# Performance work log

Hardware: AMD Instinct MI355X
Metric: run time of the kernel (lower is better)

Reference implementation:

```python
import jax, jax.numpy as jnp
import numpy as np

B, T, D_MODEL, N_HEADS = 2, 2048, 1024, 16
HEAD_DIM = D_MODEL // N_HEADS
GN_EPS = 1e-5


def decay_gammas(n_heads):
    # gamma_h = 1 - 2^(-5 - h*(8/n_heads))
    h = jnp.arange(n_heads, dtype=jnp.float32)
    return 1.0 - jnp.power(2.0, -5.0 - h * (8.0 / n_heads))


def setup_inputs() -> dict:
    key = jax.random.key(0)
    ks = jax.random.split(key, 7)
    w_scale = 0.02
    return {
        "x": jax.random.normal(ks[0], (B, T, D_MODEL), dtype=jnp.float32),
        "Wq": jax.random.normal(ks[1], (D_MODEL, D_MODEL), dtype=jnp.float32) * w_scale,
        "Wk": jax.random.normal(ks[2], (D_MODEL, D_MODEL), dtype=jnp.float32) * w_scale,
        "Wv": jax.random.normal(ks[3], (D_MODEL, D_MODEL), dtype=jnp.float32) * w_scale,
        "Wo": jax.random.normal(ks[4], (D_MODEL, D_MODEL), dtype=jnp.float32) * w_scale,
        "gn_w": jnp.ones((D_MODEL,), dtype=jnp.float32),
        "gn_b": jnp.zeros((D_MODEL,), dtype=jnp.float32),
    }


def reference(x, Wq, Wk, Wv, Wo, gn_w, gn_b):
    Bx, Tx, C = x.shape
    H, D = N_HEADS, C // N_HEADS
    gammas = decay_gammas(H)  # (H,)

    def split_heads(y):
        return y.reshape(Bx, Tx, H, D).transpose(0, 2, 1, 3)  # (B,H,T,D)

    # torch Linear: y = x @ W.T
    Q = split_heads(x @ Wq.T)
    K = split_heads(x @ Wk.T)
    V = split_heads(x @ Wv.T)

    # causal decay mask D[h,i,j] = gamma_h^(i-j) if i>=j else 0
    idx = jnp.arange(Tx, dtype=jnp.float32)
    diff = idx[:, None] - idx[None, :]  # (T,T)
    mask = jnp.where(diff >= 0,
                     gammas[:, None, None] ** jnp.maximum(diff, 0.0),
                     0.0)  # (H,T,T)

    scores = jnp.einsum("bhtd,bhsd->bhts", Q, K) / jnp.sqrt(jnp.float32(D))
    scores = scores * mask[None]  # (B,H,T,T)
    out = jnp.einsum("bhts,bhsd->bhtd", scores, V)  # (B,H,T,D)
    y = out.transpose(0, 2, 1, 3).reshape(Bx, Tx, C)  # merge heads

    # GroupNorm(n_heads, d_model) applied on (B, C, T): normalizes over
    # (head_dim, T) per group per batch element.
    z = y.transpose(0, 2, 1).reshape(Bx, H, D, Tx)
    mu = z.mean(axis=(2, 3), keepdims=True)
    var = z.var(axis=(2, 3), keepdims=True)
    zn = (z - mu) * jax.lax.rsqrt(var + GN_EPS)
    zn = zn * gn_w.reshape(1, H, D, 1) + gn_b.reshape(1, H, D, 1)
    y = zn.reshape(Bx, C, Tx).transpose(0, 2, 1)  # (B,T,C)

    return y @ Wo.T
```

## Files before the change

### kernel.cpp

```cpp
#include <hip/hip_runtime.h>
#include <hip/hip_bf16.h>

typedef __attribute__((ext_vector_type(8))) short short8;
typedef __attribute__((ext_vector_type(4))) float float4v;
typedef __attribute__((ext_vector_type(16))) float float16v;
typedef unsigned short u16;
typedef unsigned long long ull;

#define KD 1024

__device__ __forceinline__ u16 f2b(float f) {
    __hip_bfloat16 h = __float2bfloat16(f);
    return __builtin_bit_cast(u16, h);
}
__device__ __forceinline__ float b2f(u16 u) {
    unsigned x = ((unsigned)u) << 16;
    return __builtin_bit_cast(float, x);
}
__device__ __forceinline__ float lg_gamma(int h) {
    float gamma = 1.0f - exp2f(-5.0f - 0.5f * (float)h);
    return log2f(gamma);
}

__device__ __forceinline__ void async_cp16(const u16* g, u16* l) {
    __builtin_amdgcn_global_load_lds(
        (const __attribute__((address_space(1))) void*)g,
        (__attribute__((address_space(3))) void*)l,
        16, 0, 0);
}

__global__ __launch_bounds__(256)
void cvt_all(const float* __restrict__ x, const float* __restrict__ wq,
             const float* __restrict__ wk, const float* __restrict__ wv,
             const float* __restrict__ wo,
             u16* __restrict__ xb, u16* __restrict__ wqkvb, u16* __restrict__ wob)
{
    int bid = blockIdx.x;
    if (bid < 4096) {
        long i = (long)bid * 1024 + threadIdx.x * 4;
        float4 v = *(const float4*)(x + i);
        ushort4 u;
        u.x = f2b(v.x); u.y = f2b(v.y); u.z = f2b(v.z); u.w = f2b(v.w);
        *(ushort4*)(xb + i) = u;
    } else {
        int wbid = bid - 4096;
        int mtx = wbid >> 10;
        int n = wbid & 1023;
        const float* src = (mtx == 0) ? wq : (mtx == 1) ? wk : (mtx == 2) ? wv : wo;
        u16* dst = (mtx == 3) ? wob : (wqkvb + (size_t)mtx * 1048576);
        float sc = (mtx == 0) ? 0.125f : 1.0f;
        int k0 = threadIdx.x * 4;
        float4 v = *(const float4*)(src + (size_t)n * 1024 + k0);
        int panel = n >> 5, row = n & 31, kg = k0 >> 4, kh = (k0 >> 3) & 1, off = k0 & 7;
        size_t o = (size_t)panel * 32768 + (size_t)kg * 512 + kh * 256 + row * 8 + off;
        ushort4 u;
        u.x = f2b(v.x * sc); u.y = f2b(v.y * sc); u.z = f2b(v.z * sc); u.w = f2b(v.w * sc);
        *(ushort4*)(dst + o) = u;
    }
}

template<int MODE>
__global__ __launch_bounds__(256)
void gemm_nt(const u16* __restrict__ A, const u16* __restrict__ Bpk,
             u16* __restrict__ oQ, u16* __restrict__ oK,
             u16* __restrict__ oKt, u16* __restrict__ oVt,
             float* __restrict__ of)
{
    constexpr int TM = (MODE == 0) ? 128 : 64;
    constexpr int MI = (MODE == 0) ? 2 : 1;
    __shared__ __attribute__((aligned(16))) u16 Sh[(MODE == 0) ? 16384 : 4096];
    u16* As = Sh;
    const int tid = threadIdx.x;
    const int lane = tid & 63;
    const int wv = tid >> 6;
    const int wm = wv >> 1, wn = wv & 1;
    const int row32 = lane & 31, khalf = lane >> 5;
    const int lrow = lane >> 3, lseg = lane & 7;
    const int lin = blockIdx.x + gridDim.x * blockIdx.y;
    const int xcd = lin & 7, idx = lin >> 3;
    int m_tile, n_tile;
    if (MODE == 0) { m_tile = (idx & 3) + 4 * xcd; n_tile = idx >> 2; }
    else           { m_tile = (idx & 7) + 8 * xcd; n_tile = idx >> 3; }
    const int m0 = m_tile * TM, n0 = n_tile * 128;

    float16v acc[MI][2];
#pragma unroll
    for (int i = 0; i < MI; i++)
#pragma unroll
        for (int j = 0; j < 2; j++)
#pragma unroll
            for (int r = 0; r < 16; r++) acc[i][j][r] = 0.f;

    const int scol = (lseg ^ lrow) << 3;
    const u16* bp = Bpk + (size_t)((n0 >> 5) + wn * 2) * 32768 + (size_t)lane * 8;

    for (int kt = 0; kt < KD; kt += 64) {
        __syncthreads();
#pragma unroll
        for (int i = 0; i < TM / 32; i++) {
            int r = wv * (TM / 4) + i * 8;
            async_cp16(A + (size_t)(m0 + r + lrow) * KD + kt + scol, &As[r * 64]);
        }
        short8 bgl[4][2];
#pragma unroll
        for (int ks = 0; ks < 4; ks++)
#pragma unroll
            for (int j = 0; j < 2; j++)
                bgl[ks][j] = *(const short8*)(bp + (size_t)j * 32768 + ((kt >> 4) + ks) * 512);
        __syncthreads();
#pragma unroll
        for (int ks = 0; ks < 4; ks++) {
            short8 af[MI];
#pragma unroll
            for (int i = 0; i < MI; i++) {
                int row = wm * (MI * 32) + i * 32 + row32;
                af[i] = *(const short8*)(&As[row * 64 + (((ks * 2 + khalf) ^ (row & 7)) << 3)]);
            }
#pragma unroll
            for (int i = 0; i < MI; i++)
#pragma unroll
                for (int j = 0; j < 2; j++)
                    acc[i][j] = __builtin_amdgcn_mfma_f32_32x32x16_bf16(af[i], bgl[ks][j], acc[i][j], 0, 0, 0);
        }
    }

    if (MODE == 0) {
        const int wsel = n0 >> 10;
        if (wsel <= 1) {
            u16* dst = (wsel == 0) ? oQ : oK;
#pragma unroll
            for (int i = 0; i < 2; i++)
#pragma unroll
                for (int j = 0; j < 2; j++) {
                    int gn = n0 + wn * 64 + j * 32 + row32;
                    int dd = gn & 63, hh = (gn >> 6) & 15;
#pragma unroll
                    for (int reg = 0; reg < 16; reg++) {
                        int m = m0 + wm * 64 + i * 32 + (reg & 3) + 8 * (reg >> 2) + 4 * khalf;
                        int b = m >> 11, t = m & 2047;
                        dst[(size_t)(b * 16 + hh) * 131072 + t * 64 + dd] = f2b(acc[i][j][reg]);
                    }
                }
        }
        if (wsel >= 1) {
            __syncthreads();
            u16* Tl = Sh + wv * 4096;
#pragma unroll
            for (int i = 0; i < 2; i++)
#pragma unroll
                for (int j = 0; j < 2; j++) {
                    int n_loc = j * 32 + row32;
#pragma unroll
                    for (int g = 0; g < 4; g++) {
                        int m4 = i * 32 + 8 * g + 4 * khalf;
                        ull pk = (ull)f2b(acc[i][j][4 * g]) | ((ull)f2b(acc[i][j][4 * g + 1]) << 16) |
                                 ((ull)f2b(acc[i][j][4 * g + 2]) << 32) | ((ull)f2b(acc[i][j][4 * g + 3]) << 48);
                        *(ull*)(&Tl[n_loc * 64 + (((m4 >> 3) ^ (n_loc & 7)) << 3) + (m4 & 7)]) = pk;
                    }
                }
            __syncthreads();
            int gnb = n0 + wn * 64;
            int hh = (gnb >> 6) & 15;
            int mb = m0 + wm * 64;
            int bh = (mb >> 11) * 16 + hh;
            int t0 = mb & 2047;
            u16* dstT = (wsel == 1) ? oKt : oVt;
            int rr = lane >> 3, ss = lane & 7;
#pragma unroll
            for (int g = 0; g < 8; g++) {
                int row = 8 * g + rr;
                short8 v = *(const short8*)(&Tl[row * 64 + ((ss ^ rr) << 3)]);
                *(short8*)(&dstT[(size_t)bh * 131072 + (size_t)row * 2048 + t0 + ss * 8]) = v;
            }
        }
    } else {
        int gn0 = n0 + wn * 64 + row32;
#pragma unroll
        for (int g = 0; g < 4; g++)
#pragma unroll
            for (int rr = 0; rr < 4; rr++) {
                int reg = 4 * g + rr;
                int m = m0 + wm * 32 + 8 * g + 4 * khalf + rr;
                of[(size_t)m * 1024 + gn0] = acc[0][0][reg];
                of[(size_t)m * 1024 + gn0 + 32] = acc[0][1][reg];
            }
    }
}

__global__ __launch_bounds__(256)
void chunk_state(const u16* __restrict__ Kt, const u16* __restrict__ Vt,
                 u16* __restrict__ U)
{
    const int c = blockIdx.x, bh = blockIdx.y, h = bh & 15;
    const int tid = threadIdx.x, lane = tid & 63, w = tid >> 6;
    const int row16 = lane & 15, quad = lane >> 4;
    const float lg = lg_gamma(h);
    const size_t base = (size_t)bh * 131072;

    float4v acc[4];
    float4v zero4 = {0.f, 0.f, 0.f, 0.f};
#pragma unroll
    for (int tn = 0; tn < 4; tn++) acc[tn] = zero4;

#pragma unroll
    for (int kb = 0; kb < 2; kb++) {
        short8 a = *(const short8*)(Vt + base + (size_t)(16 * w + row16) * 2048 + c * 64 + kb * 32 + quad * 8);
        short8 as;
        int e0 = 63 - (kb * 32 + quad * 8);
#pragma unroll
        for (int jj = 0; jj < 8; jj++) {
            float v = b2f((u16)a[jj]) * exp2f(lg * (float)(e0 - jj));
            as[jj] = (short)f2b(v);
        }
#pragma unroll
        for (int tn = 0; tn < 4; tn++) {
            short8 bfr = *(const short8*)(Kt + base + (size_t)(16 * tn + row16) * 2048 + c * 64 + kb * 32 + quad * 8);
            acc[tn] = __builtin_amdgcn_mfma_f32_16x16x32_bf16(as, bfr, acc[tn], 0, 0, 0);
        }
    }
    u16* up = U + ((size_t)bh * 32 + c) * 4096;
#pragma unroll
    for (int tn = 0; tn < 4; tn++)
#pragma unroll
        for (int r = 0; r < 4; r++)
            up[(16 * w + quad * 4 + r) * 64 + 16 * tn + row16] = f2b(acc[tn][r]);
}

__global__ __launch_bounds__(256)
void state_scan(const u16* __restrict__ U, u16* __restrict__ St)
{
    const int bh = blockIdx.y;
    const int e = blockIdx.x * 256 + threadIdx.x;
    const float g64 = exp2f(lg_gamma(bh & 15) * 64.0f);
    float s = 0.f;
    St[(size_t)bh * 131072 + e] = 0;
    for (int c = 1; c < 32; c++) {
        s = g64 * s + b2f(U[((size_t)bh * 32 + (c - 1)) * 4096 + e]);
        St[((size_t)bh * 32 + c) * 4096 + e] = f2b(s);
    }
}

__global__ __launch_bounds__(256)
void retention_chunk(const u16* __restrict__ Q, const u16* __restrict__ Kb,
                     const u16* __restrict__ Vt, const u16* __restrict__ St,
                     float* __restrict__ Y, float* __restrict__ stats)
{
    __shared__ __attribute__((aligned(16))) u16 Pl[4][16 * 72];
    __shared__ float red[8];
    const int c = blockIdx.x, bh = blockIdx.y, h = bh & 15;
    const int tid = threadIdx.x, lane = tid & 63, w = tid >> 6;
    const int row16 = lane & 15, quad = lane >> 4;
    const float lg = lg_gamma(h);
    const size_t base = (size_t)bh * 131072;
    float4v zero4 = {0.f, 0.f, 0.f, 0.f};

    short8 qf[2];
#pragma unroll
    for (int kb = 0; kb < 2; kb++)
        qf[kb] = *(const short8*)(Q + base + (size_t)(c * 64 + 16 * w + row16) * 64 + kb * 32 + quad * 8);

    float4v accp[4];
#pragma unroll
    for (int tn = 0; tn < 4; tn++) accp[tn] = zero4;
#pragma unroll
    for (int tn = 0; tn < 4; tn++)
#pragma unroll
        for (int kb = 0; kb < 2; kb++) {
            short8 kf = *(const short8*)(Kb + base + (size_t)(c * 64 + 16 * tn + row16) * 64 + kb * 32 + quad * 8);
            accp[tn] = __builtin_amdgcn_mfma_f32_16x16x32_bf16(qf[kb], kf, accp[tn], 0, 0, 0);
        }
#pragma unroll
    for (int tn = 0; tn < 4; tn++)
#pragma unroll
        for (int r = 0; r < 4; r++) {
            int a_loc = 16 * w + quad * 4 + r;
            int b_loc = 16 * tn + row16;
            int d = a_loc - b_loc;
            float v = (d >= 0) ? accp[tn][r] * exp2f(lg * (float)d) : 0.f;
            Pl[w][(quad * 4 + r) * 72 + b_loc] = f2b(v);
        }
    __syncthreads();

    short8 pf[2];
#pragma unroll
    for (int kb = 0; kb < 2; kb++)
        pf[kb] = *(const short8*)(&Pl[w][row16 * 72 + kb * 32 + quad * 8]);

    float4v acco[4], acci[4];
#pragma unroll
    for (int tn = 0; tn < 4; tn++) { acco[tn] = zero4; acci[tn] = zero4; }
#pragma unroll
    for (int tn = 0; tn < 4; tn++)
#pragma unroll
        for (int kb = 0; kb < 2; kb++) {
            short8 vf = *(const short8*)(Vt + base + (size_t)(16 * tn + row16) * 2048 + c * 64 + kb * 32 + quad * 8);
            acco[tn] = __builtin_amdgcn_mfma_f32_16x16x32_bf16(pf[kb], vf, acco[tn], 0, 0, 0);
            short8 sf = *(const short8*)(St + ((size_t)bh * 32 + c) * 4096 + (16 * tn + row16) * 64 + kb * 32 + quad * 8);
            acci[tn] = __builtin_amdgcn_mfma_f32_16x16x32_bf16(qf[kb], sf, acci[tn], 0, 0, 0);
        }

    float s = 0.f, s2 = 0.f;
#pragma unroll
    for (int tn = 0; tn < 4; tn++)
#pragma unroll
        for (int r = 0; r < 4; r++) {
            int a_loc = 16 * w + quad * 4 + r;
            float gi = exp2f(lg * (float)(a_loc + 1));
            int t = c * 64 + a_loc, d2 = 16 * tn + row16;
            float yv = acco[tn][r] + gi * acci[tn][r];
            Y[(size_t)bh * 131072 + t * 64 + d2] = yv;
            s += yv;
            s2 += yv * yv;
        }
#pragma unroll
    for (int off = 32; off; off >>= 1) {
        s += __shfl_down(s, off, 64);
        s2 += __shfl_down(s2, off, 64);
    }
    if (lane == 0) { red[w] = s; red[4 + w] = s2; }
    __syncthreads();
    if (tid == 0) {
        atomicAdd(&stats[2 * bh], red[0] + red[1] + red[2] + red[3]);
        atomicAdd(&stats[2 * bh + 1], red[4] + red[5] + red[6] + red[7]);
    }
}

__global__ __launch_bounds__(256)
void gn_apply(const float* __restrict__ Y, const float* __restrict__ stats,
              const float* __restrict__ gnw, const float* __restrict__ gnb,
              u16* __restrict__ Z)
{
    int i4 = (blockIdx.x * 256 + threadIdx.x) * 4;
    int b = i4 >> 21, t = (i4 >> 10) & 2047, cc = i4 & 1023;
    int hh = cc >> 6, dd = cc & 63, bh = b * 16 + hh;
    float4 v = *(const float4*)(Y + (size_t)bh * 131072 + t * 64 + dd);
    float S = stats[2 * bh], S2 = stats[2 * bh + 1];
    float mu = S * (1.0f / 131072.f);
    float var = S2 * (1.0f / 131072.f) - mu * mu;
    float rsg = rsqrtf(var + 1e-5f);
    float4 wv = *(const float4*)(gnw + cc);
    float4 bv = *(const float4*)(gnb + cc);
    ushort4 o;
    o.x = f2b((v.x - mu) * rsg * wv.x + bv.x);
    o.y = f2b((v.y - mu) * rsg * wv.y + bv.y);
    o.z = f2b((v.z - mu) * rsg * wv.z + bv.z);
    o.w = f2b((v.w - mu) * rsg * wv.w + bv.w);
    *(ushort4*)(Z + i4) = o;
}

extern "C" void kernel_launch(void* const* d_in, const int* in_sizes, int n_in,
                              void* d_out, int out_size, void* d_ws, size_t ws_size,
                              hipStream_t stream) {
    const float* x   = (const float*)d_in[0];
    const float* Wq  = (const float*)d_in[1];
    const float* Wk  = (const float*)d_in[2];
    const float* Wv  = (const float*)d_in[3];
    const float* Wo  = (const float*)d_in[4];
    const float* gnw = (const float*)d_in[5];
    const float* gnb = (const float*)d_in[6];
    float* out = (float*)d_out;
    char* ws = (char*)d_ws;

    u16*  xb    = (u16*)(ws + 0);
    u16*  wqkvb = (u16*)(ws + 8388608);
    u16*  wob   = (u16*)(ws + 14680064);
    u16*  Qs    = (u16*)(ws + 16777216);
    u16*  Kb    = (u16*)(ws + 25165824);
    u16*  Kt    = (u16*)(ws + 33554432);
    u16*  Vt    = (u16*)(ws + 41943040);
    u16*  U     = (u16*)(ws + 50331648);
    u16*  St    = (u16*)(ws + 67108864);
    float* Y    = (float*)(ws + 75497472);
    u16*  Zb    = (u16*)(ws + 92274688);
    float* stats= (float*)(ws + 100663296);

    hipMemsetAsync(stats, 0, 64 * sizeof(float), stream);

    cvt_all<<<8192, 256, 0, stream>>>(x, Wq, Wk, Wv, Wo, xb, wqkvb, wob);

    gemm_nt<0><<<dim3(24, 32), 256, 0, stream>>>(xb, wqkvb, Qs, Kb, Kt, Vt, nullptr);

    chunk_state<<<dim3(32, 32), 256, 0, stream>>>(Kt, Vt, U);
    state_scan<<<dim3(16, 32), 256, 0, stream>>>(U, St);
    retention_chunk<<<dim3(32, 32), 256, 0, stream>>>(Qs, Kb, Vt, St, Y, stats);

    gn_apply<<<4096, 256, 0, stream>>>(Y, stats, gnw, gnb, Zb);

    gemm_nt<1><<<dim3(8, 64), 256, 0, stream>>>(Zb, wob, nullptr, nullptr, nullptr, nullptr, out);
}
```

Before: 185.3 us.

## Fuse state scan into retention kernel and store bf16 output in-place for GroupNorm

Removes the separate state_scan kernel. Each retention block now recomputes its prefix state by scanning all earlier chunk states U in registers and stages the result in swizzled LDS. The retention output is written as bf16 directly in (B,T,C) layout, GN statistics are taken from the rounded values, and gn_apply normalizes in place with 8-wide vectors. This saves one launch plus the fp32 Y round trip through memory, but it adds redundant scan work that grows with the chunk index, since later chunks re-read up to 31 U tiles, and it rounds Y to bf16 before normalization.

```diff
diff --git a/kernel.cpp b/kernel.cpp
--- a/kernel.cpp
+++ b/kernel.cpp
@@ -227,25 +227,12 @@
 }
 
 __global__ __launch_bounds__(256)
-void state_scan(const u16* __restrict__ U, u16* __restrict__ St)
-{
-    const int bh = blockIdx.y;
-    const int e = blockIdx.x * 256 + threadIdx.x;
-    const float g64 = exp2f(lg_gamma(bh & 15) * 64.0f);
-    float s = 0.f;
-    St[(size_t)bh * 131072 + e] = 0;
-    for (int c = 1; c < 32; c++) {
-        s = g64 * s + b2f(U[((size_t)bh * 32 + (c - 1)) * 4096 + e]);
-        St[((size_t)bh * 32 + c) * 4096 + e] = f2b(s);
-    }
-}
-
-__global__ __launch_bounds__(256)
 void retention_chunk(const u16* __restrict__ Q, const u16* __restrict__ Kb,
-                     const u16* __restrict__ Vt, const u16* __restrict__ St,
-                     float* __restrict__ Y, float* __restrict__ stats)
+                     const u16* __restrict__ Vt, const u16* __restrict__ U,
+                     u16* __restrict__ Yb, float* __restrict__ stats)
 {
     __shared__ __attribute__((aligned(16))) u16 Pl[4][16 * 72];
+    __shared__ __attribute__((aligned(16))) u16 Sl[4096];
     __shared__ float red[8];
     const int c = blockIdx.x, bh = blockIdx.y, h = bh & 15;
     const int tid = threadIdx.x, lane = tid & 63, w = tid >> 6;
@@ -259,6 +246,32 @@
     for (int kb = 0; kb < 2; kb++)
         qf[kb] = *(const short8*)(Q + base + (size_t)(c * 64 + 16 * w + row16) * 64 + kb * 32 + quad * 8);
 
+    if (c != 0) {
+        const float g64 = exp2f(lg * 64.0f);
+        float sreg[16];
+#pragma unroll
+        for (int j = 0; j < 16; j++) sreg[j] = 0.f;
+        for (int cp = 0; cp < c; cp++) {
+            const u16* up = U + ((size_t)bh * 32 + cp) * 4096 + tid * 8;
+            short8 u0 = *(const short8*)(up);
+            short8 u1 = *(const short8*)(up + 2048);
+#pragma unroll
+            for (int jj = 0; jj < 8; jj++) {
+                sreg[jj]     = g64 * sreg[jj]     + b2f((u16)u0[jj]);
+                sreg[8 + jj] = g64 * sreg[8 + jj] + b2f((u16)u1[jj]);
+            }
+        }
+#pragma unroll
+        for (int j = 0; j < 2; j++) {
+            int e0 = j * 2048 + tid * 8;
+            int row = e0 >> 6, col8 = (e0 >> 3) & 7;
+            short8 pk;
+#pragma unroll
+            for (int jj = 0; jj < 8; jj++) pk[jj] = (short)f2b(sreg[j * 8 + jj]);
+            *(short8*)(&Sl[row * 64 + ((col8 ^ (row & 7)) << 3)]) = pk;
+        }
+    }
+
     float4v accp[4];
 #pragma unroll
     for (int tn = 0; tn < 4; tn++) accp[tn] = zero4;
@@ -295,10 +308,14 @@
         for (int kb = 0; kb < 2; kb++) {
             short8 vf = *(const short8*)(Vt + base + (size_t)(16 * tn + row16) * 2048 + c * 64 + kb * 32 + quad * 8);
             acco[tn] = __builtin_amdgcn_mfma_f32_16x16x32_bf16(pf[kb], vf, acco[tn], 0, 0, 0);
-            short8 sf = *(const short8*)(St + ((size_t)bh * 32 + c) * 4096 + (16 * tn + row16) * 64 + kb * 32 + quad * 8);
-            acci[tn] = __builtin_amdgcn_mfma_f32_16x16x32_bf16(qf[kb], sf, acci[tn], 0, 0, 0);
-        }
-
+            if (c != 0) {
+                int srow = 16 * tn + row16, scol8 = kb * 4 + quad;
+                short8 sf = *(const short8*)(&Sl[srow * 64 + ((scol8 ^ (srow & 7)) << 3)]);
+                acci[tn] = __builtin_amdgcn_mfma_f32_16x16x32_bf16(qf[kb], sf, acci[tn], 0, 0, 0);
+            }
+        }
+
+    const int b = bh >> 4;
     float s = 0.f, s2 = 0.f;
 #pragma unroll
     for (int tn = 0; tn < 4; tn++)
@@ -308,9 +325,11 @@
             float gi = exp2f(lg * (float)(a_loc + 1));
             int t = c * 64 + a_loc, d2 = 16 * tn + row16;
             float yv = acco[tn][r] + gi * acci[tn][r];
-            Y[(size_t)bh * 131072 + t * 64 + d2] = yv;
-            s += yv;
-            s2 += yv * yv;
+            u16 yq = f2b(yv);
+            Yb[((size_t)(b * 2048 + t)) * 1024 + h * 64 + d2] = yq;
+            float yr = b2f(yq);
+            s += yr;
+            s2 += yr * yr;
         }
 #pragma unroll
     for (int off = 32; off; off >>= 1) {
@@ -326,26 +345,31 @@
 }
 
 __global__ __launch_bounds__(256)
-void gn_apply(const float* __restrict__ Y, const float* __restrict__ stats,
-              const float* __restrict__ gnw, const float* __restrict__ gnb,
-              u16* __restrict__ Z)
+void gn_apply(u16* __restrict__ Z, const float* __restrict__ stats,
+              const float* __restrict__ gnw, const float* __restrict__ gnb)
 {
-    int i4 = (blockIdx.x * 256 + threadIdx.x) * 4;
-    int b = i4 >> 21, t = (i4 >> 10) & 2047, cc = i4 & 1023;
-    int hh = cc >> 6, dd = cc & 63, bh = b * 16 + hh;
-    float4 v = *(const float4*)(Y + (size_t)bh * 131072 + t * 64 + dd);
+    int i8 = (blockIdx.x * 256 + threadIdx.x) * 8;
+    int b = i8 >> 21, cc = i8 & 1023;
+    int bh = b * 16 + (cc >> 6);
+    short8 v = *(const short8*)(Z + i8);
     float S = stats[2 * bh], S2 = stats[2 * bh + 1];
     float mu = S * (1.0f / 131072.f);
     float var = S2 * (1.0f / 131072.f) - mu * mu;
     float rsg = rsqrtf(var + 1e-5f);
-    float4 wv = *(const float4*)(gnw + cc);
-    float4 bv = *(const float4*)(gnb + cc);
-    ushort4 o;
-    o.x = f2b((v.x - mu) * rsg * wv.x + bv.x);
-    o.y = f2b((v.y - mu) * rsg * wv.y + bv.y);
-    o.z = f2b((v.z - mu) * rsg * wv.z + bv.z);
-    o.w = f2b((v.w - mu) * rsg * wv.w + bv.w);
-    *(ushort4*)(Z + i4) = o;
+    float4 w0 = *(const float4*)(gnw + cc);
+    float4 w1 = *(const float4*)(gnw + cc + 4);
+    float4 b0 = *(const float4*)(gnb + cc);
+    float4 b1 = *(const float4*)(gnb + cc + 4);
+    short8 o;
+    o[0] = (short)f2b((b2f((u16)v[0]) - mu) * rsg * w0.x + b0.x);
+    o[1] = (short)f2b((b2f((u16)v[1]) - mu) * rsg * w0.y + b0.y);
+    o[2] = (short)f2b((b2f((u16)v[2]) - mu) * rsg * w0.z + b0.z);
+    o[3] = (short)f2b((b2f((u16)v[3]) - mu) * rsg * w0.w + b0.w);
+    o[4] = (short)f2b((b2f((u16)v[4]) - mu) * rsg * w1.x + b1.x);
+    o[5] = (short)f2b((b2f((u16)v[5]) - mu) * rsg * w1.y + b1.y);
+    o[6] = (short)f2b((b2f((u16)v[6]) - mu) * rsg * w1.z + b1.z);
+    o[7] = (short)f2b((b2f((u16)v[7]) - mu) * rsg * w1.w + b1.w);
+    *(short8*)(Z + i8) = o;
 }
 
 extern "C" void kernel_launch(void* const* d_in, const int* in_sizes, int n_in,
@@ -369,9 +393,7 @@
     u16*  Kt    = (u16*)(ws + 33554432);
     u16*  Vt    = (u16*)(ws + 41943040);
     u16*  U     = (u16*)(ws + 50331648);
-    u16*  St    = (u16*)(ws + 67108864);
-    float* Y    = (float*)(ws + 75497472);
-    u16*  Zb    = (u16*)(ws + 92274688);
+    u16*  Yb    = (u16*)(ws + 67108864);
     float* stats= (float*)(ws + 100663296);
 
     hipMemsetAsync(stats, 0, 64 * sizeof(float), stream);
@@ -381,10 +403,9 @@
     gemm_nt<0><<<dim3(24, 32), 256, 0, stream>>>(xb, wqkvb, Qs, Kb, Kt, Vt, nullptr);
 
     chunk_state<<<dim3(32, 32), 256, 0, stream>>>(Kt, Vt, U);
-    state_scan<<<dim3(16, 32), 256, 0, stream>>>(U, St);
-    retention_chunk<<<dim3(32, 32), 256, 0, stream>>>(Qs, Kb, Vt, St, Y, stats);
-
-    gn_apply<<<4096, 256, 0, stream>>>(Y, stats, gnw, gnb, Zb);
-
-    gemm_nt<1><<<dim3(8, 64), 256, 0, stream>>>(Zb, wob, nullptr, nullptr, nullptr, nullptr, out);
-}
+    retention_chunk<<<dim3(32, 32), 256, 0, stream>>>(Qs, Kb, Vt, U, Yb, stats);
+
+    gn_apply<<<2048, 256, 0, stream>>>(Yb, stats, gnw, gnb);
+
+    gemm_nt<1><<<dim3(8, 64), 256, 0, stream>>>(Yb, wob, nullptr, nullptr, nullptr, nullptr, out);
+}
```

Result: faster. 180.8 us (-2.4%).
